# Performance work log

Hardware: AMD Instinct MI355X
Metric: run time of the kernel (lower is better)

## Reference

```python
import jax, jax.numpy as jnp
import numpy as np

UNITS = 512
NUM_HEADS = 8
QKV = UNITS // NUM_HEADS           # flax qkv_features = units // num_heads = 64
HEAD_DIM = QKV // NUM_HEADS        # flax head_dim = qkv_features // num_heads = 8
EPS = 1e-6


def layernorm(x, scale, bias):
    mu = jnp.mean(x, axis=-1, keepdims=True)
    var = jnp.mean(jnp.square(x - mu), axis=-1, keepdims=True)
    return (x - mu) * jax.lax.rsqrt(var + EPS) * scale + bias


def lstm(x, Wx, Wh, b):
    # flax nn.RNN(nn.LSTMCell): zero init carry, scan over time axis 1.
    B, T, D = x.shape
    H = Wh.shape[0]
    xg = jnp.einsum('btd,dk->btk', x, Wx) + b  # precompute input gate contributions [B,T,4H]

    def step(carry, xg_t):
        c, h = carry
        g = xg_t + h @ Wh
        i, f, gg, o = jnp.split(g, 4, axis=-1)
        c = jax.nn.sigmoid(f) * c + jax.nn.sigmoid(i) * jnp.tanh(gg)
        h = jax.nn.sigmoid(o) * jnp.tanh(c)
        return (c, h), h

    init = (jnp.zeros((B, H), x.dtype), jnp.zeros((B, H), x.dtype))
    _, hs = jax.lax.scan(step, init, jnp.swapaxes(xg, 0, 1))
    return jnp.swapaxes(hs, 0, 1)


def setup_inputs() -> dict:
    key = jax.random.key(0)
    ks = jax.random.split(key, 12)
    B, T, D = 16, 512, UNITS
    s = 0.02
    return {
        'x': jax.random.normal(ks[0], (B, T, D), jnp.float32),
        'Wx': jax.random.normal(ks[1], (D, 4 * UNITS), jnp.float32) * s,
        'Wh': jax.random.normal(ks[2], (UNITS, 4 * UNITS), jnp.float32) * s,
        'b': jnp.zeros((4 * UNITS,), jnp.float32),
        'ln1_scale': jnp.ones((UNITS,), jnp.float32),
        'ln1_bias': jnp.zeros((UNITS,), jnp.float32),
        'Wq': jax.random.normal(ks[3], (UNITS, QKV), jnp.float32) * s,
        'bq': jnp.zeros((QKV,), jnp.float32),
        'Wk': jax.random.normal(ks[4], (UNITS, QKV), jnp.float32) * s,
        'bk': jnp.zeros((QKV,), jnp.float32),
        'Wv': jax.random.normal(ks[5], (UNITS, QKV), jnp.float32) * s,
        'bv': jnp.zeros((QKV,), jnp.float32),
        'Wo': jax.random.normal(ks[6], (QKV, UNITS), jnp.float32) * s,
        'bo': jnp.zeros((UNITS,), jnp.float32),
        'Wg': jax.random.normal(ks[7], (UNITS, UNITS), jnp.float32) * s,
        'bg': jnp.zeros((UNITS,), jnp.float32),
        'ln2_scale': jnp.ones((UNITS,), jnp.float32),
        'ln2_bias': jnp.zeros((UNITS,), jnp.float32),
    }


def reference(x, Wx, Wh, b, ln1_scale, ln1_bias, Wq, bq, Wk, bk, Wv, bv, Wo, bo, Wg, bg, ln2_scale, ln2_bias):
    skip1 = x
    h = lstm(x, Wx, Wh, b)
    h = layernorm(h, ln1_scale, ln1_bias)
    h = h + skip1  # input feature dim == units, so residual applies
    skip2 = h
    B, T, _ = h.shape
    q = (h @ Wq + bq).reshape(B, T, NUM_HEADS, HEAD_DIM)
    k = (h @ Wk + bk).reshape(B, T, NUM_HEADS, HEAD_DIM)
    v = (h @ Wv + bv).reshape(B, T, NUM_HEADS, HEAD_DIM)
    scale = jnp.asarray(1.0 / np.sqrt(HEAD_DIM), h.dtype)
    scores = jnp.einsum('bqhd,bkhd->bhqk', q * scale, k)
    attn = jax.nn.softmax(scores, axis=-1)
    ctx = jnp.einsum('bhqk,bkhd->bqhd', attn, v).reshape(B, T, QKV)
    attn_out = ctx @ Wo + bo
    gate = jax.nn.sigmoid(skip2 @ Wg + bg)
    return layernorm(attn_out * gate + skip2, ln2_scale, ln2_bias)
```

## Files before the change

### kernel.cpp

```cpp
#include <hip/hip_runtime.h>

typedef unsigned short u16;
typedef unsigned int u32;
typedef unsigned long long u64;
typedef __attribute__((ext_vector_type(8))) short short8;
typedef __attribute__((ext_vector_type(4))) float f32x4;

__device__ __forceinline__ float bf2f(u16 u) {
  union { float f; unsigned int i; } x; x.i = ((unsigned int)u) << 16; return x.f;
}
__device__ __forceinline__ u16 f2bf(float f) {
  union { float f; unsigned int i; } x; x.f = f;
  unsigned int r = x.i + 0x7FFFu + ((x.i >> 16) & 1u);
  return (u16)(r >> 16);
}
__device__ __forceinline__ float sigmf(float x) { return 1.f / (1.f + __expf(-x)); }
__device__ __forceinline__ float tanhfast(float x) { return 1.f - 2.f / (__expf(2.f * x) + 1.f); }

__global__ __launch_bounds__(256) void f2bf_kernel(const float* __restrict__ src,
                                                   u16* __restrict__ dst, int n) {
  int i = blockIdx.x * 256 + threadIdx.x;
  if (i < n) dst[i] = f2bf(src[i]);
}

__global__ __launch_bounds__(256) void pack_qkv_kernel(
    const float* __restrict__ Wq, const float* __restrict__ Wk, const float* __restrict__ Wv,
    const float* __restrict__ bq, const float* __restrict__ bk, const float* __restrict__ bv,
    u16* __restrict__ Wp, float* __restrict__ bp) {
  int i = blockIdx.x * 256 + threadIdx.x;
  if (i < 512 * 192) {
    int k = i / 192, r = i % 192, s = r >> 6, c = r & 63;
    const float* W = (s == 0) ? Wq : ((s == 1) ? Wk : Wv);
    Wp[i] = f2bf(W[k * 64 + c]);
  }
  if (i < 192) {
    int s = i >> 6, c = i & 63;
    bp[i] = ((s == 0) ? bq : ((s == 1) ? bk : bv))[c];
  }
}

__global__ __launch_bounds__(256) void gemm_bf16(
    const u16* __restrict__ A, const u16* __restrict__ B, const float* __restrict__ bias,
    float* __restrict__ Cf, u16* __restrict__ Cb, int M, int N, int K, int mode) {
  __shared__ u16 As[64][72];
  __shared__ u16 Bs[64][72];
  int tid = threadIdx.x;
  int tm = blockIdx.x * 64, tn = blockIdx.y * 64;
  int w = tid >> 6, L = tid & 63, m15 = L & 15, q = L >> 4;
  int lr = tid >> 3, lk = (tid & 7) * 8;

  f32x4 zero = {0.f, 0.f, 0.f, 0.f};
  f32x4 acc[4];
#pragma unroll
  for (int j = 0; j < 4; ++j) acc[j] = zero;

  for (int tk = 0; tk < K; tk += 64) {
#pragma unroll
    for (int rr = lr; rr < 64; rr += 32) {
      short8 v = *(const short8*)(A + (size_t)(tm + rr) * K + tk + lk);
      *(short8*)&As[rr][lk] = v;
    }
#pragma unroll
    for (int rr = lr; rr < 64; rr += 32) {
      short8 v = *(const short8*)(B + (size_t)(tk + rr) * N + tn + lk);
      const short* pv = (const short*)&v;
#pragma unroll
      for (int j = 0; j < 8; ++j) Bs[lk + j][rr] = (u16)pv[j];
    }
    __syncthreads();
#pragma unroll
    for (int ks = 0; ks < 2; ++ks) {
      int k0 = ks * 32 + q * 8;
      short8 a = *(const short8*)&As[w * 16 + m15][k0];
#pragma unroll
      for (int j = 0; j < 4; ++j) {
        short8 b = *(const short8*)&Bs[j * 16 + m15][k0];
        acc[j] = __builtin_amdgcn_mfma_f32_16x16x32_bf16(a, b, acc[j], 0, 0, 0);
      }
    }
    __syncthreads();
  }
  if (mode == 2) {
    int row0 = tm + w * 16 + q * 4;
    int bq_ = row0 >> 9, t0 = row0 & 511;
#pragma unroll
    for (int j = 0; j < 4; ++j) {
      int col = tn + j * 16 + m15;
      int sel = col >> 6, cc = col & 63, hd = cc >> 3, d = cc & 7;
      float bia = bias ? bias[col] : 0.f;
      f32x4 vv;
#pragma unroll
      for (int r = 0; r < 4; ++r) vv[r] = acc[j][r] + bia;
      *(f32x4*)(Cf + ((((size_t)sel * 16 + bq_) * 8 + hd) * 8 + d) * 512 + t0) = vv;
    }
    return;
  }
#pragma unroll
  for (int j = 0; j < 4; ++j) {
    int col = tn + j * 16 + m15;
    float bia = bias ? bias[col] : 0.f;
#pragma unroll
    for (int r = 0; r < 4; ++r) {
      int row = tm + w * 16 + q * 4 + r;
      float v = acc[j][r] + bia;
      if (mode == 1) v = sigmf(v);
      if (Cf) Cf[(size_t)row * N + col] = v;
      if (Cb) Cb[(size_t)row * N + col] = f2bf(v);
    }
  }
}

__global__ __launch_bounds__(512, 2) void lstm_kernel(
    const float* __restrict__ Wh,
    const u16* __restrict__ xg,
    float* __restrict__ hs,
    u64* __restrict__ h_buf)
{
  __shared__ u16 hL[2][16][520];

  int tid = threadIdx.x;
  int wv = tid >> 6, L = tid & 63, m15 = L & 15, q = L >> 4;
  int u0w = blockIdx.x * 64 + wv * 8;

  for (int i = tid; i < 16 * 520; i += 512) ((u16*)hL[0])[i] = 0;

  short8 bfrag[16][2];
  float cst[4] = {0.f, 0.f, 0.f, 0.f};
#pragma unroll
  for (int kt = 0; kt < 16; ++kt) {
#pragma unroll
    for (int tl = 0; tl < 2; ++tl) {
      int n = tl * 16 + m15;
      int col = (n >> 3) * 512 + u0w + (n & 7);
      short8 tmp;
#pragma unroll
      for (int jj = 0; jj < 8; ++jj)
        tmp[jj] = (short)f2bf(Wh[(size_t)(kt * 32 + q * 8 + jj) * 2048 + col]);
      bfrag[kt][tl] = tmp;
    }
  }

  float xv[4][4];
  if (m15 < 8) {
#pragma unroll
    for (int r = 0; r < 4; ++r) {
      size_t base = ((size_t)((q * 4 + r) * 512)) * 2048 + u0w + m15;
#pragma unroll
      for (int g = 0; g < 4; ++g) xv[g][r] = bf2f(xg[base + g * 512]);
    }
  }
  __syncthreads();

  int p = 0;
#pragma unroll 1
  for (int t = 0; t < 512; ++t) {
    u64* hb = h_buf + (size_t)(t & 1) * 4096;

    f32x4 z = {0.f, 0.f, 0.f, 0.f};
    f32x4 a0e = z, a0o = z, a1e = z, a1o = z;
#pragma unroll
    for (int kt = 0; kt < 8; ++kt) {
      short8 aE = *(const short8*)&hL[p][m15][(2 * kt) * 32 + q * 8];
      short8 aO = *(const short8*)&hL[p][m15][(2 * kt + 1) * 32 + q * 8];
      a0e = __builtin_amdgcn_mfma_f32_16x16x32_bf16(aE, bfrag[2 * kt][0], a0e, 0, 0, 0);
      a1e = __builtin_amdgcn_mfma_f32_16x16x32_bf16(aE, bfrag[2 * kt][1], a1e, 0, 0, 0);
      a0o = __builtin_amdgcn_mfma_f32_16x16x32_bf16(aO, bfrag[2 * kt + 1][0], a0o, 0, 0, 0);
      a1o = __builtin_amdgcn_mfma_f32_16x16x32_bf16(aO, bfrag[2 * kt + 1][1], a1o, 0, 0, 0);
    }
    f32x4 acc0, acc1;
#pragma unroll
    for (int r = 0; r < 4; ++r) { acc0[r] = a0e[r] + a0o[r]; acc1[r] = a1e[r] + a1o[r]; }
    f32x4 accf, acco;
#pragma unroll
    for (int r = 0; r < 4; ++r) {
      accf[r] = __shfl_xor(acc0[r], 8);
      acco[r] = __shfl_xor(acc1[r], 8);
    }
    float hv[4] = {0.f, 0.f, 0.f, 0.f};
    unsigned int mybf[4] = {0, 0, 0, 0};
    if (m15 < 8) {
#pragma unroll
      for (int r = 0; r < 4; ++r) {
        float gi = acc0[r] + xv[0][r];
        float gf = accf[r] + xv[1][r];
        float gg = acc1[r] + xv[2][r];
        float go = acco[r] + xv[3][r];
        cst[r] = sigmf(gf) * cst[r] + sigmf(gi) * tanhfast(gg);
        hv[r] = sigmf(go) * tanhfast(cst[r]);
        mybf[r] = (unsigned int)f2bf(hv[r]);
      }
    }

    if (t == 511) {
      if (m15 < 8) {
#pragma unroll
        for (int r = 0; r < 4; ++r)
          hs[((size_t)((q * 4 + r) * 512) + t) * 512 + u0w + m15] = hv[r];
      }
      break;
    }

    unsigned int target = (unsigned int)(t + 1);
#pragma unroll
    for (int r = 0; r < 4; ++r) {
      unsigned int ob = (unsigned int)__shfl_xor((int)mybf[r], 1);
      if (m15 < 8 && (m15 & 1) == 0) {
        u64 val = ((u64)target << 32) | (u64)(mybf[r] | (ob << 16));
        __hip_atomic_store(&hb[(q * 4 + r) * 256 + ((u0w + m15) >> 1)], val,
                           __ATOMIC_RELAXED, __HIP_MEMORY_SCOPE_AGENT);
      }
    }

    u64 v[8];
#pragma unroll
    for (int j = 0; j < 8; ++j)
      v[j] = __hip_atomic_load(&hb[j * 512 + tid],
                               __ATOMIC_RELAXED, __HIP_MEMORY_SCOPE_AGENT);

    if (m15 < 8) {
#pragma unroll
      for (int r = 0; r < 4; ++r) {
        size_t base = ((size_t)((q * 4 + r) * 512 + t + 1)) * 2048 + u0w + m15;
#pragma unroll
        for (int g = 0; g < 4; ++g) xv[g][r] = bf2f(xg[base + g * 512]);
      }
#pragma unroll
      for (int r = 0; r < 4; ++r)
        hs[((size_t)((q * 4 + r) * 512) + t) * 512 + u0w + m15] = hv[r];
    }

    for (;;) {
      unsigned int need = 0;
#pragma unroll
      for (int j = 0; j < 8; ++j)
        need |= ((unsigned int)((unsigned int)(v[j] >> 32) != target)) << j;
      if (need == 0) break;
#pragma unroll
      for (int j = 0; j < 8; ++j)
        if (need & (1u << j))
          v[j] = __hip_atomic_load(&hb[j * 512 + tid],
                                   __ATOMIC_RELAXED, __HIP_MEMORY_SCOPE_AGENT);
    }

#pragma unroll
    for (int j = 0; j < 8; ++j) {
      int e = j * 512 + tid;
      *(u32*)&hL[p ^ 1][e >> 8][(e & 255) * 2] = (u32)v[j];
    }
    __syncthreads();
    p ^= 1;
  }
}

__global__ __launch_bounds__(256) void ln1_kernel(
    const float* __restrict__ hsin, const float* __restrict__ x,
    const float* __restrict__ sc, const float* __restrict__ bi,
    float* __restrict__ hF, u16* __restrict__ hB) {
  int wv = threadIdx.x >> 6, ln = threadIdx.x & 63;
  size_t row = (size_t)blockIdx.x * 4 + wv;
  size_t rb = row * 512;
  float v[8];
  float s = 0.f;
#pragma unroll
  for (int j = 0; j < 8; ++j) { v[j] = hsin[rb + ln + j * 64]; s += v[j]; }
#pragma unroll
  for (int off = 32; off; off >>= 1) s += __shfl_xor(s, off);
  float mu = s * (1.f / 512.f);
  float vs = 0.f;
#pragma unroll
  for (int j = 0; j < 8; ++j) { float d = v[j] - mu; vs += d * d; }
#pragma unroll
  for (int off = 32; off; off >>= 1) vs += __shfl_xor(vs, off);
  float rs = rsqrtf(vs * (1.f / 512.f) + 1e-6f);
#pragma unroll
  for (int j = 0; j < 8; ++j) {
    int cc = ln + j * 64;
    float y = (v[j] - mu) * rs * sc[cc] + bi[cc] + x[rb + cc];
    hF[rb + cc] = y;
    hB[rb + cc] = f2bf(y);
  }
}

__global__ __launch_bounds__(256) void ln2_kernel(
    const float* __restrict__ ao, const float* __restrict__ gate,
    const float* __restrict__ skip, const float* __restrict__ sc,
    const float* __restrict__ bi, float* __restrict__ out) {
  int wv = threadIdx.x >> 6, ln = threadIdx.x & 63;
  size_t row = (size_t)blockIdx.x * 4 + wv;
  size_t rb = row * 512;
  float v[8];
  float s = 0.f;
#pragma unroll
  for (int j = 0; j < 8; ++j) {
    size_t ix = rb + ln + j * 64;
    v[j] = ao[ix] * gate[ix] + skip[ix];
    s += v[j];
  }
#pragma unroll
  for (int off = 32; off; off >>= 1) s += __shfl_xor(s, off);
  float mu = s * (1.f / 512.f);
  float vs = 0.f;
#pragma unroll
  for (int j = 0; j < 8; ++j) { float d = v[j] - mu; vs += d * d; }
#pragma unroll
  for (int off = 32; off; off >>= 1) vs += __shfl_xor(vs, off);
  float rs = rsqrtf(vs * (1.f / 512.f) + 1e-6f);
#pragma unroll
  for (int j = 0; j < 8; ++j) {
    int cc = ln + j * 64;
    out[rb + cc] = (v[j] - mu) * rs * sc[cc] + bi[cc];
  }
}

__global__ __launch_bounds__(512) void attn_kernel(const float* __restrict__ qkvT,
                                                   u16* __restrict__ ctx) {
  __shared__ float kL[512][9];
  __shared__ float vL[512][9];
  int tid = threadIdx.x;
  int b = blockIdx.x >> 3, hd = blockIdx.x & 7;
  const float* qb = qkvT + (((size_t)0 * 16 + b) * 8 + hd) * 8 * 512;
  const float* kb = qkvT + (((size_t)1 * 16 + b) * 8 + hd) * 8 * 512;
  const float* vb = qkvT + (((size_t)2 * 16 + b) * 8 + hd) * 8 * 512;
#pragma unroll
  for (int i = tid; i < 4096; i += 512) {
    int d = i >> 9, t = i & 511;
    kL[t][d] = kb[(size_t)d * 512 + t];
    vL[t][d] = vb[(size_t)d * 512 + t];
  }
  const float scl = 0.35355339059327373f;
  float qv[8];
#pragma unroll
  for (int d = 0; d < 8; ++d) qv[d] = qb[(size_t)d * 512 + tid] * scl;
  __syncthreads();
  float m = -1e30f, l = 0.f;
  float a[8] = {0, 0, 0, 0, 0, 0, 0, 0};
  for (int t2 = 0; t2 < 512; ++t2) {
    float s = 0.f;
#pragma unroll
    for (int d = 0; d < 8; ++d) s += qv[d] * kL[t2][d];
    float nm = fmaxf(m, s);
    float cor = __expf(m - nm);
    float e = __expf(s - nm);
    l = l * cor + e;
#pragma unroll
    for (int d = 0; d < 8; ++d) a[d] = a[d] * cor + e * vL[t2][d];
    m = nm;
  }
  float inv = 1.f / l;
  short8 o;
#pragma unroll
  for (int d = 0; d < 8; ++d) o[d] = (short)f2bf(a[d] * inv);
  *(short8*)(ctx + ((size_t)b * 512 + tid) * 64 + hd * 8) = o;
}

extern "C" void kernel_launch(void* const* d_in, const int* in_sizes, int n_in,
                              void* d_out, int out_size, void* d_ws, size_t ws_size,
                              hipStream_t stream) {
  (void)in_sizes; (void)n_in; (void)out_size; (void)ws_size;
  const float* x    = (const float*)d_in[0];
  const float* Wx   = (const float*)d_in[1];
  const float* Wh   = (const float*)d_in[2];
  const float* bls  = (const float*)d_in[3];
  const float* ln1s = (const float*)d_in[4];
  const float* ln1b = (const float*)d_in[5];
  const float* Wq   = (const float*)d_in[6];
  const float* bq   = (const float*)d_in[7];
  const float* Wk   = (const float*)d_in[8];
  const float* bk   = (const float*)d_in[9];
  const float* Wv   = (const float*)d_in[10];
  const float* bv   = (const float*)d_in[11];
  const float* Wo   = (const float*)d_in[12];
  const float* bo   = (const float*)d_in[13];
  const float* Wg   = (const float*)d_in[14];
  const float* bg   = (const float*)d_in[15];
  const float* ln2s = (const float*)d_in[16];
  const float* ln2b = (const float*)d_in[17];
  float* out = (float*)d_out;

  char* p = (char*)d_ws;
  auto alloc = [&](size_t bytes) -> char* {
    char* r = p;
    p += (bytes + 255) & ~(size_t)255;
    return r;
  };
  u64* h_buf    = (u64*)alloc((size_t)2 * 4096 * 8);
  u16* x_bf     = (u16*)alloc((size_t)8192 * 512 * 2);
  u16* Wx_bf    = (u16*)alloc((size_t)512 * 2048 * 2);
  u16* Wqkv_bf  = (u16*)alloc((size_t)512 * 192 * 2);
  float* bqkv   = (float*)alloc(192 * 4);
  u16* Wg_bf    = (u16*)alloc((size_t)512 * 512 * 2);
  u16* Wo_bf    = (u16*)alloc((size_t)64 * 512 * 2);
  u16* xg_bf    = (u16*)alloc((size_t)8192 * 2048 * 2);
  float* hs     = (float*)alloc((size_t)8192 * 512 * 4);
  float* hF     = (float*)alloc((size_t)8192 * 512 * 4);
  u16* hB       = (u16*)alloc((size_t)8192 * 512 * 2);
  float* qkvT   = (float*)alloc((size_t)3 * 16 * 8 * 8 * 512 * 4);
  float* gatep  = (float*)alloc((size_t)8192 * 512 * 4);
  u16* ctx      = (u16*)alloc((size_t)8192 * 64 * 2);
  float* ao     = (float*)alloc((size_t)8192 * 512 * 4);

  f2bf_kernel<<<16384, 256, 0, stream>>>(x, x_bf, 8192 * 512);
  f2bf_kernel<<<4096, 256, 0, stream>>>(Wx, Wx_bf, 512 * 2048);
  f2bf_kernel<<<1024, 256, 0, stream>>>(Wg, Wg_bf, 512 * 512);
  f2bf_kernel<<<128, 256, 0, stream>>>(Wo, Wo_bf, 64 * 512);
  pack_qkv_kernel<<<384, 256, 0, stream>>>(Wq, Wk, Wv, bq, bk, bv, Wqkv_bf, bqkv);

  gemm_bf16<<<dim3(128, 32), 256, 0, stream>>>(x_bf, Wx_bf, bls, nullptr, xg_bf,
                                               8192, 2048, 512, 0);
  lstm_kernel<<<8, 512, 0, stream>>>(Wh, xg_bf, hs, h_buf);
  ln1_kernel<<<2048, 256, 0, stream>>>(hs, x, ln1s, ln1b, hF, hB);
  gemm_bf16<<<dim3(128, 3), 256, 0, stream>>>(hB, Wqkv_bf, bqkv, qkvT, nullptr,
                                              8192, 192, 512, 2);
  gemm_bf16<<<dim3(128, 8), 256, 0, stream>>>(hB, Wg_bf, bg, gatep, nullptr,
                                              8192, 512, 512, 1);
  attn_kernel<<<128, 512, 0, stream>>>(qkvT, ctx);
  gemm_bf16<<<dim3(128, 8), 256, 0, stream>>>(ctx, Wo_bf, bo, ao, nullptr,
                                              8192, 512, 64, 0);
  ln2_kernel<<<2048, 256, 0, stream>>>(ao, gatep, hF, ln2s, ln2b, out);
}
```

Before: 2.833 ms.

## Elect one XCD for LSTM blocks so the cross-block handshake stays in one L2

Launches 64 LSTM blocks and has each read its XCC id from a hardware register. The first XCC to gather eight blocks is elected, its eight blocks run the recurrence, and all other blocks exit; a timeout falls back to using block ids. The goal is to keep the per-timestep h exchange between the eight cooperating blocks inside one XCD's L2 instead of crossing dies. The polling loop now uses inline-asm global loads with the sc0 cache bit, moves the hs stores ahead of the loads, and sleeps after six failed rounds. The election depends on an undocumented hwreg layout and on spin timing, which adds startup cost and a risk of deadlock.

```diff
diff --git a/kernel.cpp b/kernel.cpp
--- a/kernel.cpp
+++ b/kernel.cpp
@@ -114,13 +114,49 @@
     const float* __restrict__ Wh,
     const u16* __restrict__ xg,
     float* __restrict__ hs,
-    u64* __restrict__ h_buf)
+    u64* __restrict__ h_buf,
+    int* __restrict__ elect)
 {
   __shared__ u16 hL[2][16][520];
+  __shared__ int role_s;
 
   int tid = threadIdx.x;
+
+  if (tid == 0) {
+    unsigned int xcc;
+    asm volatile("s_getreg_b32 %0, hwreg(20, 0, 32)" : "=s"(xcc));
+    xcc &= 7u;
+    int rank = __hip_atomic_fetch_add(&elect[1 + xcc], 1,
+                                      __ATOMIC_RELAXED, __HIP_MEMORY_SCOPE_AGENT);
+    if (rank == 7) {
+      int exp0 = 0;
+      __hip_atomic_compare_exchange_strong(
+          &elect[0], &exp0, (int)xcc + 1,
+          __ATOMIC_RELAXED, __ATOMIC_RELAXED, __HIP_MEMORY_SCOPE_AGENT);
+    }
+    int w, iter = 0;
+    for (;;) {
+      w = __hip_atomic_load(&elect[0], __ATOMIC_RELAXED, __HIP_MEMORY_SCOPE_AGENT);
+      if (w != 0) break;
+      if (++iter > 20000) {
+        int exp0 = 0;
+        __hip_atomic_compare_exchange_strong(
+            &elect[0], &exp0, 9,
+            __ATOMIC_RELAXED, __ATOMIC_RELAXED, __HIP_MEMORY_SCOPE_AGENT);
+      }
+      __builtin_amdgcn_s_sleep(2);
+    }
+    if (w == 9)
+      role_s = (blockIdx.x < 8) ? (int)blockIdx.x : -1;
+    else
+      role_s = ((int)xcc == w - 1 && rank < 8) ? rank : -1;
+  }
+  __syncthreads();
+  int g = role_s;
+  if (g < 0) return;
+
   int wv = tid >> 6, L = tid & 63, m15 = L & 15, q = L >> 4;
-  int u0w = blockIdx.x * 64 + wv * 8;
+  int u0w = g * 64 + wv * 8;
 
   for (int i = tid; i < 16 * 520; i += 512) ((u16*)hL[0])[i] = 0;
 
@@ -146,7 +182,7 @@
     for (int r = 0; r < 4; ++r) {
       size_t base = ((size_t)((q * 4 + r) * 512)) * 2048 + u0w + m15;
 #pragma unroll
-      for (int g = 0; g < 4; ++g) xv[g][r] = bf2f(xg[base + g * 512]);
+      for (int gg2 = 0; gg2 < 4; ++gg2) xv[gg2][r] = bf2f(xg[base + gg2 * 512]);
     }
   }
   __syncthreads();
@@ -211,35 +247,53 @@
       }
     }
 
-    u64 v[8];
-#pragma unroll
-    for (int j = 0; j < 8; ++j)
-      v[j] = __hip_atomic_load(&hb[j * 512 + tid],
-                               __ATOMIC_RELAXED, __HIP_MEMORY_SCOPE_AGENT);
-
     if (m15 < 8) {
+#pragma unroll
+      for (int r = 0; r < 4; ++r)
+        hs[((size_t)((q * 4 + r) * 512) + t) * 512 + u0w + m15] = hv[r];
 #pragma unroll
       for (int r = 0; r < 4; ++r) {
         size_t base = ((size_t)((q * 4 + r) * 512 + t + 1)) * 2048 + u0w + m15;
 #pragma unroll
-        for (int g = 0; g < 4; ++g) xv[g][r] = bf2f(xg[base + g * 512]);
-      }
-#pragma unroll
-      for (int r = 0; r < 4; ++r)
-        hs[((size_t)((q * 4 + r) * 512) + t) * 512 + u0w + m15] = hv[r];
-    }
-
+        for (int gg2 = 0; gg2 < 4; ++gg2) xv[gg2][r] = bf2f(xg[base + gg2 * 512]);
+      }
+    }
+
+    u64 v[8];
+#pragma unroll
+    for (int j = 0; j < 8; ++j) {
+      const u64* ap = hb + j * 512 + tid;
+      asm volatile("global_load_dwordx2 %0, %1, off sc0"
+                   : "=v"(v[j]) : "v"(ap) : "memory");
+    }
+    asm volatile("s_waitcnt vmcnt(0)" ::: "memory");
+
+    int rounds = 0;
     for (;;) {
       unsigned int need = 0;
 #pragma unroll
       for (int j = 0; j < 8; ++j)
         need |= ((unsigned int)((unsigned int)(v[j] >> 32) != target)) << j;
       if (need == 0) break;
-#pragma unroll
-      for (int j = 0; j < 8; ++j)
-        if (need & (1u << j))
-          v[j] = __hip_atomic_load(&hb[j * 512 + tid],
-                                   __ATOMIC_RELAXED, __HIP_MEMORY_SCOPE_AGENT);
+      ++rounds;
+      if (rounds <= 6) {
+#pragma unroll
+        for (int j = 0; j < 8; ++j) {
+          if (need & (1u << j)) {
+            const u64* ap = hb + j * 512 + tid;
+            asm volatile("global_load_dwordx2 %0, %1, off sc0"
+                         : "=v"(v[j]) : "v"(ap) : "memory");
+          }
+        }
+        asm volatile("s_waitcnt vmcnt(0)" ::: "memory");
+      } else {
+        __builtin_amdgcn_s_sleep(1);
+#pragma unroll
+        for (int j = 0; j < 8; ++j)
+          if (need & (1u << j))
+            v[j] = __hip_atomic_load(&hb[j * 512 + tid],
+                                     __ATOMIC_RELAXED, __HIP_MEMORY_SCOPE_AGENT);
+      }
     }
 
 #pragma unroll
@@ -383,6 +437,7 @@
     p += (bytes + 255) & ~(size_t)255;
     return r;
   };
+  int* elect    = (int*)alloc(16 * 4);
   u64* h_buf    = (u64*)alloc((size_t)2 * 4096 * 8);
   u16* x_bf     = (u16*)alloc((size_t)8192 * 512 * 2);
   u16* Wx_bf    = (u16*)alloc((size_t)512 * 2048 * 2);
@@ -399,6 +454,7 @@
   u16* ctx      = (u16*)alloc((size_t)8192 * 64 * 2);
   float* ao     = (float*)alloc((size_t)8192 * 512 * 4);
 
+  hipMemsetAsync(elect, 0, 16 * 4, stream);
   f2bf_kernel<<<16384, 256, 0, stream>>>(x, x_bf, 8192 * 512);
   f2bf_kernel<<<4096, 256, 0, stream>>>(Wx, Wx_bf, 512 * 2048);
   f2bf_kernel<<<1024, 256, 0, stream>>>(Wg, Wg_bf, 512 * 512);
@@ -407,7 +463,7 @@
 
   gemm_bf16<<<dim3(128, 32), 256, 0, stream>>>(x_bf, Wx_bf, bls, nullptr, xg_bf,
                                                8192, 2048, 512, 0);
-  lstm_kernel<<<8, 512, 0, stream>>>(Wh, xg_bf, hs, h_buf);
+  lstm_kernel<<<64, 512, 0, stream>>>(Wh, xg_bf, hs, h_buf, elect);
   ln1_kernel<<<2048, 256, 0, stream>>>(hs, x, ln1s, ln1b, hF, hB);
   gemm_bf16<<<dim3(128, 3), 256, 0, stream>>>(hB, Wqkv_bf, bqkv, qkvT, nullptr,
                                               8192, 192, 512, 2);
```

New measurement: 3.945 ms. 39.3% more time.

## Load LSTM hidden state straight into MFMA fragments, dropping LDS staging and barrier

Applied to the files above, without the earlier changes.

Each wave now reads the flagged hidden-state words it needs from the global exchange buffer directly in MFMA A-fragment layout. Loads and spin-waits run chunk by chunk, double-buffered, so matrix multiplies on arrived chunks overlap waiting for later ones. This removes the shared-memory staging copy and the per-step __syncthreads. It adds fixed s_sleep delays before polling and a sleep inside the spin loop, which may add latency per timestep, and each wave now issues its own redundant global loads.

```diff
diff --git a/kernel.cpp b/kernel.cpp
--- a/kernel.cpp
+++ b/kernel.cpp
@@ -116,13 +116,9 @@
     float* __restrict__ hs,
     u64* __restrict__ h_buf)
 {
-  __shared__ u16 hL[2][16][520];
-
   int tid = threadIdx.x;
   int wv = tid >> 6, L = tid & 63, m15 = L & 15, q = L >> 4;
   int u0w = blockIdx.x * 64 + wv * 8;
-
-  for (int i = tid; i < 16 * 520; i += 512) ((u16*)hL[0])[i] = 0;
 
   short8 bfrag[16][2];
   float cst[4] = {0.f, 0.f, 0.f, 0.f};
@@ -146,27 +142,15 @@
     for (int r = 0; r < 4; ++r) {
       size_t base = ((size_t)((q * 4 + r) * 512)) * 2048 + u0w + m15;
 #pragma unroll
-      for (int g = 0; g < 4; ++g) xv[g][r] = bf2f(xg[base + g * 512]);
-    }
-  }
-  __syncthreads();
-
-  int p = 0;
+      for (int g2 = 0; g2 < 4; ++g2) xv[g2][r] = bf2f(xg[base + g2 * 512]);
+    }
+  }
+
+  f32x4 z = {0.f, 0.f, 0.f, 0.f};
+  f32x4 a0e = z, a0o = z, a1e = z, a1o = z;
+
 #pragma unroll 1
   for (int t = 0; t < 512; ++t) {
-    u64* hb = h_buf + (size_t)(t & 1) * 4096;
-
-    f32x4 z = {0.f, 0.f, 0.f, 0.f};
-    f32x4 a0e = z, a0o = z, a1e = z, a1o = z;
-#pragma unroll
-    for (int kt = 0; kt < 8; ++kt) {
-      short8 aE = *(const short8*)&hL[p][m15][(2 * kt) * 32 + q * 8];
-      short8 aO = *(const short8*)&hL[p][m15][(2 * kt + 1) * 32 + q * 8];
-      a0e = __builtin_amdgcn_mfma_f32_16x16x32_bf16(aE, bfrag[2 * kt][0], a0e, 0, 0, 0);
-      a1e = __builtin_amdgcn_mfma_f32_16x16x32_bf16(aE, bfrag[2 * kt][1], a1e, 0, 0, 0);
-      a0o = __builtin_amdgcn_mfma_f32_16x16x32_bf16(aO, bfrag[2 * kt + 1][0], a0o, 0, 0, 0);
-      a1o = __builtin_amdgcn_mfma_f32_16x16x32_bf16(aO, bfrag[2 * kt + 1][1], a1o, 0, 0, 0);
-    }
     f32x4 acc0, acc1;
 #pragma unroll
     for (int r = 0; r < 4; ++r) { acc0[r] = a0e[r] + a0o[r]; acc1[r] = a1e[r] + a1o[r]; }
@@ -191,64 +175,85 @@
       }
     }
 
-    if (t == 511) {
-      if (m15 < 8) {
-#pragma unroll
-        for (int r = 0; r < 4; ++r)
-          hs[((size_t)((q * 4 + r) * 512) + t) * 512 + u0w + m15] = hv[r];
-      }
-      break;
-    }
-
+    u64* hb = h_buf + (size_t)(t & 1) * 4096;
     unsigned int target = (unsigned int)(t + 1);
-#pragma unroll
-    for (int r = 0; r < 4; ++r) {
-      unsigned int ob = (unsigned int)__shfl_xor((int)mybf[r], 1);
-      if (m15 < 8 && (m15 & 1) == 0) {
-        u64 val = ((u64)target << 32) | (u64)(mybf[r] | (ob << 16));
-        __hip_atomic_store(&hb[(q * 4 + r) * 256 + ((u0w + m15) >> 1)], val,
-                           __ATOMIC_RELAXED, __HIP_MEMORY_SCOPE_AGENT);
-      }
-    }
-
-    u64 v[8];
-#pragma unroll
-    for (int j = 0; j < 8; ++j)
-      v[j] = __hip_atomic_load(&hb[j * 512 + tid],
-                               __ATOMIC_RELAXED, __HIP_MEMORY_SCOPE_AGENT);
+
+    if (t < 511) {
+#pragma unroll
+      for (int r = 0; r < 4; ++r) {
+        unsigned int ob = (unsigned int)__shfl_xor((int)mybf[r], 1);
+        if (m15 < 8 && (m15 & 1) == 0) {
+          u64 val = ((u64)target << 32) | (u64)(mybf[r] | (ob << 16));
+          __hip_atomic_store(&hb[(q * 4 + r) * 256 + ((u0w + m15) >> 1)], val,
+                             __ATOMIC_RELAXED, __HIP_MEMORY_SCOPE_AGENT);
+        }
+      }
+    }
 
     if (m15 < 8) {
-#pragma unroll
-      for (int r = 0; r < 4; ++r) {
-        size_t base = ((size_t)((q * 4 + r) * 512 + t + 1)) * 2048 + u0w + m15;
-#pragma unroll
-        for (int g = 0; g < 4; ++g) xv[g][r] = bf2f(xg[base + g * 512]);
-      }
 #pragma unroll
       for (int r = 0; r < 4; ++r)
         hs[((size_t)((q * 4 + r) * 512) + t) * 512 + u0w + m15] = hv[r];
-    }
-
-    for (;;) {
-      unsigned int need = 0;
-#pragma unroll
-      for (int j = 0; j < 8; ++j)
-        need |= ((unsigned int)((unsigned int)(v[j] >> 32) != target)) << j;
-      if (need == 0) break;
-#pragma unroll
-      for (int j = 0; j < 8; ++j)
-        if (need & (1u << j))
-          v[j] = __hip_atomic_load(&hb[j * 512 + tid],
+      if (t < 511) {
+#pragma unroll
+        for (int r = 0; r < 4; ++r) {
+          size_t base = ((size_t)((q * 4 + r) * 512 + t + 1)) * 2048 + u0w + m15;
+#pragma unroll
+          for (int g2 = 0; g2 < 4; ++g2) xv[g2][r] = bf2f(xg[base + g2 * 512]);
+        }
+      }
+    }
+    if (t == 511) break;
+
+    __builtin_amdgcn_s_sleep(12);
+    __builtin_amdgcn_s_sleep(12);
+
+    a0e = z; a0o = z; a1e = z; a1o = z;
+    const u64* gb = hb + m15 * 256 + q * 4;
+    u64 vb[2][8];
+#pragma unroll
+    for (int j = 0; j < 8; ++j)
+      vb[0][j] = __hip_atomic_load(&gb[(j >> 2) * 16 + (j & 3)],
                                    __ATOMIC_RELAXED, __HIP_MEMORY_SCOPE_AGENT);
-    }
-
-#pragma unroll
-    for (int j = 0; j < 8; ++j) {
-      int e = j * 512 + tid;
-      *(u32*)&hL[p ^ 1][e >> 8][(e & 255) * 2] = (u32)v[j];
-    }
-    __syncthreads();
-    p ^= 1;
+#pragma unroll
+    for (int c = 0; c < 8; ++c) {
+      if (c < 7) {
+#pragma unroll
+        for (int j = 0; j < 8; ++j)
+          vb[(c + 1) & 1][j] = __hip_atomic_load(
+              &gb[((c + 1) * 2 + (j >> 2)) * 16 + (j & 3)],
+              __ATOMIC_RELAXED, __HIP_MEMORY_SCOPE_AGENT);
+      }
+      for (;;) {
+        unsigned int need = 0;
+#pragma unroll
+        for (int j = 0; j < 8; ++j)
+          need |= ((unsigned int)((unsigned int)(vb[c & 1][j] >> 32) != target)) << j;
+        if (need == 0) break;
+        __builtin_amdgcn_s_sleep(1);
+#pragma unroll
+        for (int j = 0; j < 8; ++j)
+          if (need & (1u << j))
+            vb[c & 1][j] = __hip_atomic_load(
+                &gb[(c * 2 + (j >> 2)) * 16 + (j & 3)],
+                __ATOMIC_RELAXED, __HIP_MEMORY_SCOPE_AGENT);
+      }
+#pragma unroll
+      for (int g2 = 0; g2 < 2; ++g2) {
+        int kt = c * 2 + g2;
+        short8 a;
+        u32* ap = (u32*)&a;
+#pragma unroll
+        for (int j = 0; j < 4; ++j) ap[j] = (u32)vb[c & 1][g2 * 4 + j];
+        if (kt & 1) {
+          a0o = __builtin_amdgcn_mfma_f32_16x16x32_bf16(a, bfrag[kt][0], a0o, 0, 0, 0);
+          a1o = __builtin_amdgcn_mfma_f32_16x16x32_bf16(a, bfrag[kt][1], a1o, 0, 0, 0);
+        } else {
+          a0e = __builtin_amdgcn_mfma_f32_16x16x32_bf16(a, bfrag[kt][0], a0e, 0, 0, 0);
+          a1e = __builtin_amdgcn_mfma_f32_16x16x32_bf16(a, bfrag[kt][1], a1e, 0, 0, 0);
+        }
+      }
+    }
   }
 }
 
```

Result: slower. 10.48 ms (+270.0%).

## Split LSTM batch into two interleaved halves to overlap cross-block exchange with compute

Applied to the files above, without the earlier changes.

The persistent LSTM kernel now splits the 16-sequence batch into two groups of 8 and alternates between them over 1024 half-steps. While one group's MFMA recurrent matmul runs, the block waits on and gathers the other group's hidden state from the global exchange buffer, so inter-block latency is hidden behind compute. The cost is that each half-step uses only half of the MFMA M dimension (rows 8-15 duplicate 0-7), and the number of barriers doubles. A short s_sleep is added to the spin-wait loop.

```diff
diff --git a/kernel.cpp b/kernel.cpp
--- a/kernel.cpp
+++ b/kernel.cpp
@@ -116,16 +116,15 @@
     float* __restrict__ hs,
     u64* __restrict__ h_buf)
 {
-  __shared__ u16 hL[2][16][520];
+  __shared__ u16 hL[2][8][520];
 
   int tid = threadIdx.x;
   int wv = tid >> 6, L = tid & 63, m15 = L & 15, q = L >> 4;
   int u0w = blockIdx.x * 64 + wv * 8;
 
-  for (int i = tid; i < 16 * 520; i += 512) ((u16*)hL[0])[i] = 0;
+  for (int i = tid; i < 2 * 8 * 520 / 2; i += 512) ((u32*)hL)[i] = 0;
 
   short8 bfrag[16][2];
-  float cst[4] = {0.f, 0.f, 0.f, 0.f};
 #pragma unroll
   for (int kt = 0; kt < 16; ++kt) {
 #pragma unroll
@@ -140,33 +139,64 @@
     }
   }
 
-  float xv[4][4];
-  if (m15 < 8) {
-#pragma unroll
-    for (int r = 0; r < 4; ++r) {
-      size_t base = ((size_t)((q * 4 + r) * 512)) * 2048 + u0w + m15;
-#pragma unroll
-      for (int g = 0; g < 4; ++g) xv[g][r] = bf2f(xg[base + g * 512]);
-    }
+  float cst[2][4] = {{0.f, 0.f, 0.f, 0.f}, {0.f, 0.f, 0.f, 0.f}};
+  float xv[2][4][4];
+  if (q < 2 && m15 < 8) {
+#pragma unroll
+    for (int X = 0; X < 2; ++X)
+#pragma unroll
+      for (int r = 0; r < 4; ++r) {
+        size_t base = ((size_t)((X * 8 + q * 4 + r) * 512)) * 2048 + u0w + m15;
+#pragma unroll
+        for (int g2 = 0; g2 < 4; ++g2) xv[X][g2][r] = bf2f(xg[base + g2 * 512]);
+      }
   }
   __syncthreads();
 
-  int p = 0;
+  u64 vb[4];
 #pragma unroll 1
-  for (int t = 0; t < 512; ++t) {
-    u64* hb = h_buf + (size_t)(t & 1) * 4096;
+  for (int m = 0; m < 1024; ++m) {
+    int X = m & 1, s = m >> 1;
 
     f32x4 z = {0.f, 0.f, 0.f, 0.f};
     f32x4 a0e = z, a0o = z, a1e = z, a1o = z;
 #pragma unroll
     for (int kt = 0; kt < 8; ++kt) {
-      short8 aE = *(const short8*)&hL[p][m15][(2 * kt) * 32 + q * 8];
-      short8 aO = *(const short8*)&hL[p][m15][(2 * kt + 1) * 32 + q * 8];
+      short8 aE = *(const short8*)&hL[m & 1][m15 & 7][(2 * kt) * 32 + q * 8];
+      short8 aO = *(const short8*)&hL[m & 1][m15 & 7][(2 * kt + 1) * 32 + q * 8];
       a0e = __builtin_amdgcn_mfma_f32_16x16x32_bf16(aE, bfrag[2 * kt][0], a0e, 0, 0, 0);
       a1e = __builtin_amdgcn_mfma_f32_16x16x32_bf16(aE, bfrag[2 * kt][1], a1e, 0, 0, 0);
       a0o = __builtin_amdgcn_mfma_f32_16x16x32_bf16(aO, bfrag[2 * kt + 1][0], a0o, 0, 0, 0);
       a1o = __builtin_amdgcn_mfma_f32_16x16x32_bf16(aO, bfrag[2 * kt + 1][1], a1o, 0, 0, 0);
     }
+
+    if (m >= 1) {
+      int sY = (m - 1) >> 1;
+      if (sY < 511) {
+        int Y = (m - 1) & 1;
+        u64* hbY = h_buf + ((size_t)Y * 2 + (sY & 1)) * 2048;
+        unsigned int tgt = (unsigned int)(sY + 1);
+        for (;;) {
+          unsigned int need = 0;
+#pragma unroll
+          for (int j = 0; j < 4; ++j)
+            need |= ((unsigned int)((unsigned int)(vb[j] >> 32) != tgt)) << j;
+          if (need == 0) break;
+          __builtin_amdgcn_s_sleep(1);
+#pragma unroll
+          for (int j = 0; j < 4; ++j)
+            if (need & (1u << j))
+              vb[j] = __hip_atomic_load(&hbY[j * 512 + tid],
+                                        __ATOMIC_RELAXED, __HIP_MEMORY_SCOPE_AGENT);
+        }
+#pragma unroll
+        for (int j = 0; j < 4; ++j) {
+          int e = j * 512 + tid;
+          *(u32*)&hL[(m + 1) & 1][e >> 8][(e & 255) * 2] = (u32)vb[j];
+        }
+      }
+    }
+
     f32x4 acc0, acc1;
 #pragma unroll
     for (int r = 0; r < 4; ++r) { acc0[r] = a0e[r] + a0o[r]; acc1[r] = a1e[r] + a1o[r]; }
@@ -178,77 +208,51 @@
     }
     float hv[4] = {0.f, 0.f, 0.f, 0.f};
     unsigned int mybf[4] = {0, 0, 0, 0};
-    if (m15 < 8) {
+    if (q < 2 && m15 < 8) {
 #pragma unroll
       for (int r = 0; r < 4; ++r) {
-        float gi = acc0[r] + xv[0][r];
-        float gf = accf[r] + xv[1][r];
-        float gg = acc1[r] + xv[2][r];
-        float go = acco[r] + xv[3][r];
-        cst[r] = sigmf(gf) * cst[r] + sigmf(gi) * tanhfast(gg);
-        hv[r] = sigmf(go) * tanhfast(cst[r]);
+        float gi = acc0[r] + xv[X][0][r];
+        float gf = accf[r] + xv[X][1][r];
+        float gg = acc1[r] + xv[X][2][r];
+        float go = acco[r] + xv[X][3][r];
+        cst[X][r] = sigmf(gf) * cst[X][r] + sigmf(gi) * tanhfast(gg);
+        hv[r] = sigmf(go) * tanhfast(cst[X][r]);
         mybf[r] = (unsigned int)f2bf(hv[r]);
       }
     }
 
-    if (t == 511) {
-      if (m15 < 8) {
-#pragma unroll
-        for (int r = 0; r < 4; ++r)
-          hs[((size_t)((q * 4 + r) * 512) + t) * 512 + u0w + m15] = hv[r];
-      }
-      break;
-    }
-
-    unsigned int target = (unsigned int)(t + 1);
-#pragma unroll
-    for (int r = 0; r < 4; ++r) {
-      unsigned int ob = (unsigned int)__shfl_xor((int)mybf[r], 1);
-      if (m15 < 8 && (m15 & 1) == 0) {
-        u64 val = ((u64)target << 32) | (u64)(mybf[r] | (ob << 16));
-        __hip_atomic_store(&hb[(q * 4 + r) * 256 + ((u0w + m15) >> 1)], val,
-                           __ATOMIC_RELAXED, __HIP_MEMORY_SCOPE_AGENT);
-      }
-    }
-
-    u64 v[8];
-#pragma unroll
-    for (int j = 0; j < 8; ++j)
-      v[j] = __hip_atomic_load(&hb[j * 512 + tid],
-                               __ATOMIC_RELAXED, __HIP_MEMORY_SCOPE_AGENT);
-
-    if (m15 < 8) {
+    u64* hbX = h_buf + ((size_t)X * 2 + (s & 1)) * 2048;
+    if (s < 511) {
+      unsigned int target = (unsigned int)(s + 1);
 #pragma unroll
       for (int r = 0; r < 4; ++r) {
-        size_t base = ((size_t)((q * 4 + r) * 512 + t + 1)) * 2048 + u0w + m15;
-#pragma unroll
-        for (int g = 0; g < 4; ++g) xv[g][r] = bf2f(xg[base + g * 512]);
-      }
+        unsigned int ob = (unsigned int)__shfl_xor((int)mybf[r], 1);
+        if (q < 2 && m15 < 8 && (m15 & 1) == 0) {
+          u64 val = ((u64)target << 32) | (u64)(mybf[r] | (ob << 16));
+          __hip_atomic_store(&hbX[(q * 4 + r) * 256 + ((u0w + m15) >> 1)], val,
+                             __ATOMIC_RELAXED, __HIP_MEMORY_SCOPE_AGENT);
+        }
+      }
+#pragma unroll
+      for (int j = 0; j < 4; ++j)
+        vb[j] = __hip_atomic_load(&hbX[j * 512 + tid],
+                                  __ATOMIC_RELAXED, __HIP_MEMORY_SCOPE_AGENT);
+    }
+
+    if (q < 2 && m15 < 8) {
 #pragma unroll
       for (int r = 0; r < 4; ++r)
-        hs[((size_t)((q * 4 + r) * 512) + t) * 512 + u0w + m15] = hv[r];
-    }
-
-    for (;;) {
-      unsigned int need = 0;
-#pragma unroll
-      for (int j = 0; j < 8; ++j)
-        need |= ((unsigned int)((unsigned int)(v[j] >> 32) != target)) << j;
-      if (need == 0) break;
-#pragma unroll
-      for (int j = 0; j < 8; ++j)
-        if (need & (1u << j))
-          v[j] = __hip_atomic_load(&hb[j * 512 + tid],
-                                   __ATOMIC_RELAXED, __HIP_MEMORY_SCOPE_AGENT);
-    }
-
-#pragma unroll
-    for (int j = 0; j < 8; ++j) {
-      int e = j * 512 + tid;
-      *(u32*)&hL[p ^ 1][e >> 8][(e & 255) * 2] = (u32)v[j];
+        hs[((size_t)((X * 8 + q * 4 + r) * 512) + s) * 512 + u0w + m15] = hv[r];
+      if (s + 1 < 512) {
+#pragma unroll
+        for (int r = 0; r < 4; ++r) {
+          size_t base = ((size_t)((X * 8 + q * 4 + r) * 512 + s + 1)) * 2048 + u0w + m15;
+#pragma unroll
+          for (int g2 = 0; g2 < 4; ++g2) xv[X][g2][r] = bf2f(xg[base + g2 * 512]);
+        }
+      }
     }
     __syncthreads();
-    p ^= 1;
   }
 }
 
@@ -383,7 +387,7 @@
     p += (bytes + 255) & ~(size_t)255;
     return r;
   };
-  u64* h_buf    = (u64*)alloc((size_t)2 * 4096 * 8);
+  u64* h_buf    = (u64*)alloc((size_t)2 * 2 * 2048 * 8);
   u16* x_bf     = (u16*)alloc((size_t)8192 * 512 * 2);
   u16* Wx_bf    = (u16*)alloc((size_t)512 * 2048 * 2);
   u16* Wqkv_bf  = (u16*)alloc((size_t)512 * 192 * 2);
```

After: 7.663 ms. 2.71x slower.
